# Optimization experiments

Hardware: AMD Instinct MI355X
Metric: run time of the kernel (lower is better)

The kernel has to match this reference:

```python
import jax, jax.numpy as jnp
import numpy as np

N = 50000   # nodes
E = 640000  # edges
IN = 128
HID = 128
EPS = 1e-5


def setup_inputs() -> dict:
    key = jax.random.key(0)
    ks = jax.random.split(key, 8)
    s = 1.0 / np.sqrt(IN)
    inp = {
        "x": jax.random.normal(ks[0], (N, IN), jnp.float32),
        "src": jax.random.randint(ks[1], (E,), 0, N, dtype=jnp.int32),
        "dst": jax.random.randint(ks[2], (E,), 0, N, dtype=jnp.int32),
        "W1": jax.random.normal(ks[3], (IN, HID), jnp.float32) * s,
        "b1": jnp.zeros((HID,), jnp.float32),
        "g1": jnp.ones((HID,), jnp.float32),
        "be1": jnp.zeros((HID,), jnp.float32),
        "W2": jax.random.normal(ks[4], (HID, HID), jnp.float32) * s,
        "b2": jnp.zeros((HID,), jnp.float32),
        "g2": jnp.ones((HID,), jnp.float32),
        "be2": jnp.zeros((HID,), jnp.float32),
        "W3": jax.random.normal(ks[5], (HID, HID), jnp.float32) * s,
        "b3": jnp.zeros((HID,), jnp.float32),
        "g3": jnp.ones((HID,), jnp.float32),
        "be3": jnp.zeros((HID,), jnp.float32),
    }
    return inp


def _layernorm(h, g, b):
    mu = jnp.mean(h, axis=-1, keepdims=True)
    var = jnp.mean(jnp.square(h - mu), axis=-1, keepdims=True)
    return g * (h - mu) * jax.lax.rsqrt(var + EPS) + b


def _gcn_conv(h, W, b, src, dst):
    # Kipf & Welling GCN: D^{-1/2} (A + I) D^{-1/2} (H W) + b
    # self-loops added with weight 1; degree computed on the target index.
    hw = h @ W                                          # [N, HID]
    deg = jax.ops.segment_sum(jnp.ones((E,), h.dtype), dst, num_segments=N) + 1.0
    dinv = jax.lax.rsqrt(deg)                           # deg >= 1 due to self loop
    msg = hw[src] * (dinv[src] * dinv[dst])[:, None]    # gather + normalize, [E, HID]
    agg = jax.ops.segment_sum(msg, dst, num_segments=N)  # scatter-add
    agg = agg + hw * (dinv * dinv)[:, None]             # self-loop contribution
    return agg + b


def reference(x, src, dst, W1, b1, g1, be1, W2, b2, g2, be2, W3, b3, g3, be3):
    layers = [(W1, b1, g1, be1), (W2, b2, g2, be2), (W3, b3, g3, be3)]
    h = x
    for i, (W, b, g, be) in enumerate(layers):
        h_in = h
        h = _gcn_conv(h, W, b, src, dst)
        h = _layernorm(h, g, be)
        h = jax.nn.relu(h)
        # dropout: eval mode -> identity
        if i > 0 and h.shape == h_in.shape:
            h = h + h_in
    return h
```

## Files before the change

### kernel.cpp

```cpp
#include <hip/hip_runtime.h>
#include <hip/hip_bf16.h>

#define NFEAT 128
#define EPSLN 1e-5f
#define PAD 48

typedef __attribute__((ext_vector_type(8))) short short8;
typedef __attribute__((ext_vector_type(4))) float f32x4;

__device__ __forceinline__ float bf2f(ushort u) {
    union { uint u32; float f; } v; v.u32 = ((uint)u) << 16; return v.f;
}
__device__ __forceinline__ ushort f2bf(float f) {
    union { float f; uint u32; } v; v.f = f;
    uint u = v.u32;
    u += 0x7FFF + ((u >> 16) & 1);
    return (ushort)(u >> 16);
}

__global__ void setup_kernel(int4* __restrict__ cnt4, int ncnt4,
                             ushort* __restrict__ hwb_padrow,
                             const float* __restrict__ W0, const float* __restrict__ W1,
                             const float* __restrict__ W2,
                             ushort* __restrict__ Wt0, ushort* __restrict__ Wt1,
                             ushort* __restrict__ Wt2) {
    int i = blockIdx.x * 256 + threadIdx.x;
    if (i < ncnt4) cnt4[i] = make_int4(0, 0, 0, 0);
    if (i < 16) ((uint4*)hwb_padrow)[i] = make_uint4(0, 0, 0, 0);
    if (i < 3 * NFEAT * NFEAT) {
        int l = i / (NFEAT * NFEAT);
        int r = i - l * (NFEAT * NFEAT);
        int k = r >> 7, n = r & 127;
        const float* W = (l == 0) ? W0 : (l == 1) ? W1 : W2;
        ushort* Wt = (l == 0) ? Wt0 : (l == 1) ? Wt1 : Wt2;
        Wt[n * NFEAT + k] = f2bf(W[r]);
    }
}

__global__ void fill_kernel(const int* __restrict__ src, const int* __restrict__ dst,
                            int* __restrict__ cnt, int* __restrict__ csr, int E) {
    int e = blockIdx.x * 256 + threadIdx.x;
    if (e < E) {
        int d = dst[e];
        int s = src[e];
        int pos = atomicAdd(&cnt[d], 1);
        if (pos < PAD) csr[d * PAD + pos] = s;
    }
}

__global__ __launch_bounds__(256) void gemm_mfma_kernel(const ushort* __restrict__ hb,
                                                        const float* __restrict__ hf,
                                                        const ushort* __restrict__ Wt,
                                                        const int* __restrict__ cnt,
                                                        ushort* __restrict__ hw, int N) {
    __shared__ ushort WtL[NFEAT * NFEAT];
    {
        const uint4* src4 = (const uint4*)Wt;
        uint4* dst4 = (uint4*)WtL;
        #pragma unroll
        for (int i = 0; i < 8; ++i)
            dst4[threadIdx.x + i * 256] = src4[threadIdx.x + i * 256];
    }
    __syncthreads();

    const int wave = threadIdx.x >> 6;
    const int lane = threadIdx.x & 63;
    const int quad = lane >> 4;
    const int l16  = lane & 15;
    const int row0 = blockIdx.x * 128 + wave * 32;

    short8 afrag[2][4];
    #pragma unroll
    for (int t = 0; t < 2; ++t) {
        const int arow = row0 + t * 16 + l16;
        const bool rowok = (arow < N);
        if (hf) {
            const float4* fp = (const float4*)(hf + (size_t)arow * NFEAT);
            #pragma unroll
            for (int ks = 0; ks < 4; ++ks) {
                short8 a = short8{0, 0, 0, 0, 0, 0, 0, 0};
                if (rowok) {
                    float4 u0 = fp[ks * 8 + quad * 2];
                    float4 u1 = fp[ks * 8 + quad * 2 + 1];
                    a[0] = (short)f2bf(u0.x); a[1] = (short)f2bf(u0.y);
                    a[2] = (short)f2bf(u0.z); a[3] = (short)f2bf(u0.w);
                    a[4] = (short)f2bf(u1.x); a[5] = (short)f2bf(u1.y);
                    a[6] = (short)f2bf(u1.z); a[7] = (short)f2bf(u1.w);
                }
                afrag[t][ks] = a;
            }
        } else {
            const short8* ap = (const short8*)(hb + (size_t)arow * NFEAT);
            #pragma unroll
            for (int ks = 0; ks < 4; ++ks) {
                if (rowok) afrag[t][ks] = ap[ks * 4 + quad];
                else       afrag[t][ks] = short8{0, 0, 0, 0, 0, 0, 0, 0};
            }
        }
    }

    f32x4 acc[2][8];
    #pragma unroll
    for (int t = 0; t < 2; ++t)
        #pragma unroll
        for (int ct = 0; ct < 8; ++ct) acc[t][ct] = f32x4{0.f, 0.f, 0.f, 0.f};

    #pragma unroll
    for (int ct = 0; ct < 8; ++ct) {
        const int bcol = ct * 16 + l16;
        const short8* bp = (const short8*)(WtL + (size_t)bcol * NFEAT);
        #pragma unroll
        for (int ks = 0; ks < 4; ++ks) {
            short8 bfrag = bp[ks * 4 + quad];
            acc[0][ct] = __builtin_amdgcn_mfma_f32_16x16x32_bf16(afrag[0][ks], bfrag, acc[0][ct], 0, 0, 0);
            acc[1][ct] = __builtin_amdgcn_mfma_f32_16x16x32_bf16(afrag[1][ks], bfrag, acc[1][ct], 0, 0, 0);
        }
    }

    __syncthreads();
    ushort* tb = WtL + wave * (32 * NFEAT);

    #pragma unroll
    for (int t = 0; t < 2; ++t) {
        #pragma unroll
        for (int r = 0; r < 4; ++r) {
            const int rl = t * 16 + quad * 4 + r;
            const int orow = row0 + rl;
            const float di = (orow < N) ? rsqrtf((float)cnt[orow] + 1.0f) : 0.f;
            #pragma unroll
            for (int ct = 0; ct < 8; ++ct)
                tb[rl * NFEAT + ct * 16 + l16] = f2bf(acc[t][ct][r] * di);
        }
    }
    #pragma unroll
    for (int i = 0; i < 8; ++i) {
        const int c = i * 64 + lane;
        const int rl = c >> 4;
        const int ch = c & 15;
        const int orow = row0 + rl;
        uint4 v = *(const uint4*)(tb + rl * NFEAT + ch * 8);
        if (orow < N)
            ((uint4*)(hw + (size_t)orow * NFEAT))[ch] = v;
    }
}

__global__ __launch_bounds__(256) void agg_ln_kernel(const ushort* __restrict__ hwb,
                                                     const int* __restrict__ cnt,
                                                     const int* __restrict__ csr,
                                                     const float* __restrict__ bias,
                                                     const float* __restrict__ gamma,
                                                     const float* __restrict__ beta,
                                                     const ushort* __restrict__ hres_b,
                                                     float* __restrict__ outf,
                                                     ushort* __restrict__ outb,
                                                     int N) {
    const int lane = threadIdx.x & 63;
    const int wave = threadIdx.x >> 6;
    const int grp  = lane >> 4;
    const int l16  = lane & 15;
    const int c0i  = l16 * 8;

    int node = blockIdx.x * 16 + wave * 4 + grp;
    const bool ok = (node < N);
    if (!ok) node = N - 1;

    const int* ce = csr + (size_t)node * PAD;
    const uint4* hw4 = (const uint4*)hwb;

    const int cl = (l16 < 12) ? l16 : 11;
    int4 myidx4 = ((const int4*)ce)[cl];
    const int cn = cnt[node];
    uint4 hv = hw4[(size_t)node * 16 + l16];
    uint4 hr = make_uint4(0, 0, 0, 0);
    if (hres_b) hr = ((const uint4*)hres_b)[(size_t)node * 16 + l16];

    const int deg = (cn < PAD) ? cn : PAD;

    int ng = (deg + 3) >> 2;
    { int t = __shfl_xor(ng, 16); ng = (t > ng) ? t : ng; }
    { int t = __shfl_xor(ng, 32); ng = (t > ng) ? t : ng; }

    float acc[8];
    #pragma unroll
    for (int i = 0; i < 8; ++i) acc[i] = 0.f;

    const int grpbase = lane & 48;

#define ACC4(vv)                                                    \
    do {                                                            \
        acc[0] += bf2f((ushort)((vv).x & 0xFFFF));                  \
        acc[1] += bf2f((ushort)((vv).x >> 16));                     \
        acc[2] += bf2f((ushort)((vv).y & 0xFFFF));                  \
        acc[3] += bf2f((ushort)((vv).y >> 16));                     \
        acc[4] += bf2f((ushort)((vv).z & 0xFFFF));                  \
        acc[5] += bf2f((ushort)((vv).z >> 16));                     \
        acc[6] += bf2f((ushort)((vv).w & 0xFFFF));                  \
        acc[7] += bf2f((ushort)((vv).w >> 16));                     \
    } while (0)

    uint4 v0, v1, v2, v3;
    {
        int t0 = __shfl(myidx4.x, grpbase);
        int t1 = __shfl(myidx4.y, grpbase);
        int t2 = __shfl(myidx4.z, grpbase);
        int t3 = __shfl(myidx4.w, grpbase);
        const int s0 = (0 < deg) ? t0 : N;
        const int s1 = (1 < deg) ? t1 : N;
        const int s2 = (2 < deg) ? t2 : N;
        const int s3 = (3 < deg) ? t3 : N;
        v0 = hw4[(size_t)s0 * 16 + l16];
        v1 = hw4[(size_t)s1 * 16 + l16];
        v2 = hw4[(size_t)s2 * 16 + l16];
        v3 = hw4[(size_t)s3 * 16 + l16];
    }

    for (int it = 0; it + 1 < ng; ++it) {
        const int sl = grpbase + it + 1;
        int t0 = __shfl(myidx4.x, sl);
        int t1 = __shfl(myidx4.y, sl);
        int t2 = __shfl(myidx4.z, sl);
        int t3 = __shfl(myidx4.w, sl);
        const int e0 = (it + 1) * 4;
        const int s0 = (e0     < deg) ? t0 : N;
        const int s1 = (e0 + 1 < deg) ? t1 : N;
        const int s2 = (e0 + 2 < deg) ? t2 : N;
        const int s3 = (e0 + 3 < deg) ? t3 : N;
        uint4 w0 = hw4[(size_t)s0 * 16 + l16];
        uint4 w1 = hw4[(size_t)s1 * 16 + l16];
        uint4 w2 = hw4[(size_t)s2 * 16 + l16];
        uint4 w3 = hw4[(size_t)s3 * 16 + l16];
        ACC4(v0); ACC4(v1); ACC4(v2); ACC4(v3);
        v0 = w0; v1 = w1; v2 = w2; v3 = w3;
    }
    ACC4(v0); ACC4(v1); ACC4(v2); ACC4(v3);
#undef ACC4

    const float di = rsqrtf((float)cn + 1.0f);

    float4 b0 = ((const float4*)(bias + c0i))[0];
    float4 b1 = ((const float4*)(bias + c0i))[1];
    float xv[8];
    xv[0] = (acc[0] + bf2f((ushort)(hv.x & 0xFFFF))) * di + b0.x;
    xv[1] = (acc[1] + bf2f((ushort)(hv.x >> 16)))   * di + b0.y;
    xv[2] = (acc[2] + bf2f((ushort)(hv.y & 0xFFFF))) * di + b0.z;
    xv[3] = (acc[3] + bf2f((ushort)(hv.y >> 16)))   * di + b0.w;
    xv[4] = (acc[4] + bf2f((ushort)(hv.z & 0xFFFF))) * di + b1.x;
    xv[5] = (acc[5] + bf2f((ushort)(hv.z >> 16)))   * di + b1.y;
    xv[6] = (acc[6] + bf2f((ushort)(hv.w & 0xFFFF))) * di + b1.z;
    xv[7] = (acc[7] + bf2f((ushort)(hv.w >> 16)))   * di + b1.w;

    float s = 0.f, sq = 0.f;
    #pragma unroll
    for (int i = 0; i < 8; ++i) { s += xv[i]; sq += xv[i] * xv[i]; }
    #pragma unroll
    for (int o = 8; o > 0; o >>= 1) {
        s  += __shfl_xor(s, o);
        sq += __shfl_xor(sq, o);
    }
    const float mu  = s * (1.0f / NFEAT);
    const float var = sq * (1.0f / NFEAT) - mu * mu;
    const float rs  = rsqrtf(var + EPSLN);

    float4 g0 = ((const float4*)(gamma + c0i))[0];
    float4 g1 = ((const float4*)(gamma + c0i))[1];
    float4 e0 = ((const float4*)(beta + c0i))[0];
    float4 e1 = ((const float4*)(beta + c0i))[1];
    float gm[8] = {g0.x, g0.y, g0.z, g0.w, g1.x, g1.y, g1.z, g1.w};
    float bt[8] = {e0.x, e0.y, e0.z, e0.w, e1.x, e1.y, e1.z, e1.w};

    float y[8];
    #pragma unroll
    for (int i = 0; i < 8; ++i)
        y[i] = fmaxf(gm[i] * (xv[i] - mu) * rs + bt[i], 0.0f);

    if (hres_b) {
        y[0] += bf2f((ushort)(hr.x & 0xFFFF));
        y[1] += bf2f((ushort)(hr.x >> 16));
        y[2] += bf2f((ushort)(hr.y & 0xFFFF));
        y[3] += bf2f((ushort)(hr.y >> 16));
        y[4] += bf2f((ushort)(hr.z & 0xFFFF));
        y[5] += bf2f((ushort)(hr.z >> 16));
        y[6] += bf2f((ushort)(hr.w & 0xFFFF));
        y[7] += bf2f((ushort)(hr.w >> 16));
    }

    if (ok) {
        if (outf) {
            float4* op = (float4*)(outf + (size_t)node * NFEAT + c0i);
            op[0] = make_float4(y[0], y[1], y[2], y[3]);
            op[1] = make_float4(y[4], y[5], y[6], y[7]);
        }
        if (outb) {
            uint4 ob;
            ob.x = (uint)f2bf(y[0]) | ((uint)f2bf(y[1]) << 16);
            ob.y = (uint)f2bf(y[2]) | ((uint)f2bf(y[3]) << 16);
            ob.z = (uint)f2bf(y[4]) | ((uint)f2bf(y[5]) << 16);
            ob.w = (uint)f2bf(y[6]) | ((uint)f2bf(y[7]) << 16);
            ((uint4*)outb)[(size_t)node * 16 + l16] = ob;
        }
    }
}

extern "C" void kernel_launch(void* const* d_in, const int* in_sizes, int n_in,
                              void* d_out, int out_size, void* d_ws, size_t ws_size,
                              hipStream_t stream) {
    const float* x   = (const float*)d_in[0];
    const int*   src = (const int*)d_in[1];
    const int*   dst = (const int*)d_in[2];
    const float* W[3]  = {(const float*)d_in[3], (const float*)d_in[7],  (const float*)d_in[11]};
    const float* b[3]  = {(const float*)d_in[4], (const float*)d_in[8],  (const float*)d_in[12]};
    const float* g[3]  = {(const float*)d_in[5], (const float*)d_in[9],  (const float*)d_in[13]};
    const float* be[3] = {(const float*)d_in[6], (const float*)d_in[10], (const float*)d_in[14]};

    const int N = in_sizes[0] / NFEAT;
    const int E = in_sizes[1];

    char* ws = (char*)d_ws;
    size_t off = 0;
    auto carve = [&](size_t bytes) -> char* {
        char* p = ws + off;
        off = (off + bytes + 255) & ~(size_t)255;
        return p;
    };
    const int ncnt4 = (N + 3) / 4;
    int*    cnt = (int*)   carve((size_t)ncnt4 * 4 * sizeof(int));
    int*    csr = (int*)   carve(((size_t)N * PAD + 64) * sizeof(int));
    ushort* hwb = (ushort*)carve((size_t)(N + 1) * NFEAT * sizeof(ushort));
    ushort* h1b = (ushort*)carve((size_t)N * NFEAT * sizeof(ushort));
    ushort* h2b = (ushort*)carve((size_t)N * NFEAT * sizeof(ushort));
    ushort* Wt[3];
    for (int l = 0; l < 3; ++l) Wt[l] = (ushort*)carve(NFEAT * NFEAT * sizeof(ushort));
    (void)ws_size;

    int setup_threads = 3 * NFEAT * NFEAT;
    if (ncnt4 > setup_threads) setup_threads = ncnt4;
    setup_kernel<<<(setup_threads + 255) / 256, 256, 0, stream>>>(
        (int4*)cnt, ncnt4, hwb + (size_t)N * NFEAT,
        W[0], W[1], W[2], Wt[0], Wt[1], Wt[2]);

    fill_kernel<<<(E + 255) / 256, 256, 0, stream>>>(src, dst, cnt, csr, E);

    const ushort* hbin[3]  = {nullptr, h1b, h2b};
    const float*  hfin[3]  = {x, nullptr, nullptr};
    const ushort* hresb[3] = {nullptr, h1b, h2b};
    float*        houtf[3] = {nullptr, nullptr, (float*)d_out};
    ushort*       houtb[3] = {h1b, h2b, nullptr};

    const int gemm_blocks = (N + 127) / 128;
    const int agg_blocks = (N + 15) / 16;

    for (int l = 0; l < 3; ++l) {
        gemm_mfma_kernel<<<gemm_blocks, 256, 0, stream>>>(hbin[l], hfin[l], Wt[l], cnt, hwb, N);
        agg_ln_kernel<<<agg_blocks, 256, 0, stream>>>(hwb, cnt, csr,
                                                      b[l], g[l], be[l],
                                                      hresb[l], houtf[l], houtb[l], N);
    }
}
```

Measured before the change: 256.7 us.

## Permute feature layout to store GEMM output rows directly without LDS staging

Stores intermediate activations in a permuted feature order (feature f at position (f%16)*8+f/16). Each MFMA lane can then pack its 8 column-tile results into one 16-byte store, which removes the LDS transpose and its barrier in the GEMM epilogue. Weights and the bias, gamma and beta vectors are pre-permuted in setup to match. The cost is strided scalar loads of the fp32 input in layer 1 and strided scalar stores of the final fp32 output to undo the permutation.

```diff
diff --git a/kernel.cpp b/kernel.cpp
--- a/kernel.cpp
+++ b/kernel.cpp
@@ -7,6 +7,7 @@
 
 typedef __attribute__((ext_vector_type(8))) short short8;
 typedef __attribute__((ext_vector_type(4))) float f32x4;
+
 
 __device__ __forceinline__ float bf2f(ushort u) {
     union { uint u32; float f; } v; v.u32 = ((uint)u) << 16; return v.f;
@@ -23,7 +24,11 @@
                              const float* __restrict__ W0, const float* __restrict__ W1,
                              const float* __restrict__ W2,
                              ushort* __restrict__ Wt0, ushort* __restrict__ Wt1,
-                             ushort* __restrict__ Wt2) {
+                             ushort* __restrict__ Wt2,
+                             const float* __restrict__ b0, const float* __restrict__ g0, const float* __restrict__ be0,
+                             const float* __restrict__ b1, const float* __restrict__ g1, const float* __restrict__ be1,
+                             const float* __restrict__ b2, const float* __restrict__ g2, const float* __restrict__ be2,
+                             float* __restrict__ pprm) {
     int i = blockIdx.x * 256 + threadIdx.x;
     if (i < ncnt4) cnt4[i] = make_int4(0, 0, 0, 0);
     if (i < 16) ((uint4*)hwb_padrow)[i] = make_uint4(0, 0, 0, 0);
@@ -31,9 +36,19 @@
         int l = i / (NFEAT * NFEAT);
         int r = i - l * (NFEAT * NFEAT);
         int k = r >> 7, n = r & 127;
+        int p = (k & 15) * 8 + (k >> 4);
         const float* W = (l == 0) ? W0 : (l == 1) ? W1 : W2;
         ushort* Wt = (l == 0) ? Wt0 : (l == 1) ? Wt1 : Wt2;
-        Wt[n * NFEAT + k] = f2bf(W[r]);
+        Wt[n * NFEAT + p] = f2bf(W[r]);
+    }
+    if (i < 3 * 384) {
+        int l = i / 384, q = i - l * 384;
+        int vec = q >> 7, p = q & 127;
+        int f = (p & 7) * 16 + (p >> 3);
+        const float* s = (l == 0) ? (vec == 0 ? b0 : vec == 1 ? g0 : be0)
+                       : (l == 1) ? (vec == 0 ? b1 : vec == 1 ? g1 : be1)
+                                  : (vec == 0 ? b2 : vec == 1 ? g2 : be2);
+        pprm[i] = s[f];
     }
 }
 
@@ -75,17 +90,15 @@
         const int arow = row0 + t * 16 + l16;
         const bool rowok = (arow < N);
         if (hf) {
-            const float4* fp = (const float4*)(hf + (size_t)arow * NFEAT);
+            const float* fp = hf + (size_t)arow * NFEAT;
             #pragma unroll
             for (int ks = 0; ks < 4; ++ks) {
                 short8 a = short8{0, 0, 0, 0, 0, 0, 0, 0};
                 if (rowok) {
-                    float4 u0 = fp[ks * 8 + quad * 2];
-                    float4 u1 = fp[ks * 8 + quad * 2 + 1];
-                    a[0] = (short)f2bf(u0.x); a[1] = (short)f2bf(u0.y);
-                    a[2] = (short)f2bf(u0.z); a[3] = (short)f2bf(u0.w);
-                    a[4] = (short)f2bf(u1.x); a[5] = (short)f2bf(u1.y);
-                    a[6] = (short)f2bf(u1.z); a[7] = (short)f2bf(u1.w);
+                    const int c = ks * 4 + quad;
+                    #pragma unroll
+                    for (int j = 0; j < 8; ++j)
+                        a[j] = (short)f2bf(fp[j * 16 + c]);
                 }
                 afrag[t][ks] = a;
             }
@@ -117,30 +130,21 @@
         }
     }
 
-    __syncthreads();
-    ushort* tb = WtL + wave * (32 * NFEAT);
-
     #pragma unroll
     for (int t = 0; t < 2; ++t) {
         #pragma unroll
         for (int r = 0; r < 4; ++r) {
-            const int rl = t * 16 + quad * 4 + r;
-            const int orow = row0 + rl;
-            const float di = (orow < N) ? rsqrtf((float)cnt[orow] + 1.0f) : 0.f;
-            #pragma unroll
-            for (int ct = 0; ct < 8; ++ct)
-                tb[rl * NFEAT + ct * 16 + l16] = f2bf(acc[t][ct][r] * di);
-        }
-    }
-    #pragma unroll
-    for (int i = 0; i < 8; ++i) {
-        const int c = i * 64 + lane;
-        const int rl = c >> 4;
-        const int ch = c & 15;
-        const int orow = row0 + rl;
-        uint4 v = *(const uint4*)(tb + rl * NFEAT + ch * 8);
-        if (orow < N)
-            ((uint4*)(hw + (size_t)orow * NFEAT))[ch] = v;
+            const int orow = row0 + t * 16 + quad * 4 + r;
+            if (orow < N) {
+                const float di = rsqrtf((float)cnt[orow] + 1.0f);
+                uint4 o;
+                o.x = (uint)f2bf(acc[t][0][r] * di) | ((uint)f2bf(acc[t][1][r] * di) << 16);
+                o.y = (uint)f2bf(acc[t][2][r] * di) | ((uint)f2bf(acc[t][3][r] * di) << 16);
+                o.z = (uint)f2bf(acc[t][4][r] * di) | ((uint)f2bf(acc[t][5][r] * di) << 16);
+                o.w = (uint)f2bf(acc[t][6][r] * di) | ((uint)f2bf(acc[t][7][r] * di) << 16);
+                ((uint4*)(hw + (size_t)orow * NFEAT))[l16] = o;
+            }
+        }
     }
 }
 
@@ -286,9 +290,10 @@
 
     if (ok) {
         if (outf) {
-            float4* op = (float4*)(outf + (size_t)node * NFEAT + c0i);
-            op[0] = make_float4(y[0], y[1], y[2], y[3]);
-            op[1] = make_float4(y[4], y[5], y[6], y[7]);
+            float* op = outf + (size_t)node * NFEAT + l16;
+            #pragma unroll
+            for (int j = 0; j < 8; ++j)
+                op[j * 16] = y[j];
         }
         if (outb) {
             uint4 ob;
@@ -330,13 +335,15 @@
     ushort* h2b = (ushort*)carve((size_t)N * NFEAT * sizeof(ushort));
     ushort* Wt[3];
     for (int l = 0; l < 3; ++l) Wt[l] = (ushort*)carve(NFEAT * NFEAT * sizeof(ushort));
+    float* pprm = (float*)carve(3 * 384 * sizeof(float));
     (void)ws_size;
 
     int setup_threads = 3 * NFEAT * NFEAT;
     if (ncnt4 > setup_threads) setup_threads = ncnt4;
     setup_kernel<<<(setup_threads + 255) / 256, 256, 0, stream>>>(
         (int4*)cnt, ncnt4, hwb + (size_t)N * NFEAT,
-        W[0], W[1], W[2], Wt[0], Wt[1], Wt[2]);
+        W[0], W[1], W[2], Wt[0], Wt[1], Wt[2],
+        b[0], g[0], be[0], b[1], g[1], be[1], b[2], g[2], be[2], pprm);
 
     fill_kernel<<<(E + 255) / 256, 256, 0, stream>>>(src, dst, cnt, csr, E);
 
@@ -352,7 +359,7 @@
     for (int l = 0; l < 3; ++l) {
         gemm_mfma_kernel<<<gemm_blocks, 256, 0, stream>>>(hbin[l], hfin[l], Wt[l], cnt, hwb, N);
         agg_ln_kernel<<<agg_blocks, 256, 0, stream>>>(hwb, cnt, csr,
-                                                      b[l], g[l], be[l],
+                                                      pprm + l * 384, pprm + l * 384 + 128, pprm + l * 384 + 256,
                                                       hresb[l], houtf[l], houtb[l], N);
     }
 }
```

Result: slower. 262.8 us (+2.4%).
